# Kernel tuning notes

Hardware: AMD Instinct MI355X
Metric: run time of the kernel (lower is better)

The kernel has to match this reference:

```python
import jax, jax.numpy as jnp
import numpy as np

N = 50000      # nodes
E = 800000     # edges (before self-loops)
V = 50000      # vocab
D = 128        # embed_dim
H = 128        # hidden_dim
G = 64         # graphs in batch


def setup_inputs() -> dict:
    key = jax.random.key(0)
    ks = jax.random.split(key, 14)
    x_lex = jax.random.randint(ks[0], (N,), 0, V)
    edge_index = jax.random.randint(ks[1], (2, E), 0, N)
    batch = jnp.sort(jax.random.randint(ks[2], (N,), 0, G))
    s = 1.0 / np.sqrt(D)
    emb = jax.random.normal(ks[3], (V, D), dtype=jnp.float32) * s
    W1 = jax.random.normal(ks[4], (D, H), dtype=jnp.float32) * s
    att_src1 = jax.random.normal(ks[5], (H,), dtype=jnp.float32) * s
    att_dst1 = jax.random.normal(ks[6], (H,), dtype=jnp.float32) * s
    b1 = jnp.zeros((H,), dtype=jnp.float32)
    W2 = jax.random.normal(ks[7], (H, H), dtype=jnp.float32) * s
    att_src2 = jax.random.normal(ks[8], (H,), dtype=jnp.float32) * s
    att_dst2 = jax.random.normal(ks[9], (H,), dtype=jnp.float32) * s
    b2 = jnp.zeros((H,), dtype=jnp.float32)
    Wc = jax.random.normal(ks[10], (H, 1), dtype=jnp.float32) * s
    bc = jnp.zeros((1,), dtype=jnp.float32)
    return dict(x_lex=x_lex, edge_index=edge_index, batch=batch, emb=emb,
                W1=W1, att_src1=att_src1, att_dst1=att_dst1, b1=b1,
                W2=W2, att_src2=att_src2, att_dst2=att_dst2, b2=b2,
                Wc=Wc, bc=bc)


def _gat_conv(x, src, dst, W, a_src, a_dst, b):
    # PyG GATConv, heads=1, self-loops already appended to src/dst.
    h = x @ W                                   # [N, H]
    e = jax.nn.leaky_relu((h @ a_src)[src] + (h @ a_dst)[dst], 0.2)  # [Etot]
    m = jax.ops.segment_max(e, dst, num_segments=N)
    p = jnp.exp(e - m[dst])
    z = jax.ops.segment_sum(p, dst, num_segments=N)
    alpha = p / z[dst]                          # softmax per destination node
    out = jax.ops.segment_sum(alpha[:, None] * h[src], dst, num_segments=N)
    return out + b


def reference(x_lex, edge_index, batch, emb, W1, att_src1, att_dst1, b1,
              W2, att_src2, att_dst2, b2, Wc, bc):
    loops = jnp.arange(N, dtype=edge_index.dtype)
    src = jnp.concatenate([edge_index[0], loops])   # add self-loops (PyG default)
    dst = jnp.concatenate([edge_index[1], loops])
    x = emb[x_lex]                                  # [N, D]
    h = jax.nn.relu(_gat_conv(x, src, dst, W1, att_src1, att_dst1, b1))
    h = jax.nn.relu(_gat_conv(h, src, dst, W2, att_src2, att_dst2, b2))
    sums = jax.ops.segment_sum(h, batch, num_segments=G)           # [G, H]
    cnt = jax.ops.segment_sum(jnp.ones((N,), h.dtype), batch, num_segments=G)
    h_pool = sums / jnp.maximum(cnt, 1.0)[:, None]
    logits = h_pool @ Wc + bc                                       # [G, 1]
    return (logits, h_pool)
```

## Files before the change

kernel.cpp:

```cpp
#include <hip/hip_runtime.h>
#include <hip/hip_bf16.h>


#define THREADS 256
#define PSLICE 16
#define BUK_S 196
#define SORT_BLOCKS 128

typedef __attribute__((ext_vector_type(8))) short short8v;
typedef __attribute__((ext_vector_type(4))) float f32x4;

static __device__ __forceinline__ unsigned short f2bf(float f) {
    unsigned int u = __float_as_uint(f);
    return (unsigned short)((u + 0x7fffu + ((u >> 16) & 1u)) >> 16);
}
static __device__ __forceinline__ float bf2f(unsigned short b) {
    return __uint_as_float(((unsigned int)b) << 16);
}

__global__ __launch_bounds__(THREADS) void k_prep(const float* __restrict__ W1,
                                                  const float* __restrict__ W2,
                                                  unsigned short* __restrict__ Wh1,
                                                  unsigned short* __restrict__ Wl1,
                                                  unsigned short* __restrict__ Wh2,
                                                  unsigned short* __restrict__ Wl2,
                                                  int* __restrict__ bcount, int nbuk) {
    if (blockIdx.x == 0 && threadIdx.x < nbuk) bcount[threadIdx.x] = 0;
    int t = blockIdx.x * THREADS + threadIdx.x;
    const float* W = W1;
    unsigned short* Wh = Wh1;
    unsigned short* Wl = Wl1;
    if (t >= 128 * 128) {
        t -= 128 * 128;
        W = W2; Wh = Wh2; Wl = Wl2;
    }
    int k = t >> 7, n = t & 127;
    float w = W[t];
    unsigned short h = f2bf(w);
    unsigned short lo = f2bf(w - bf2f(h));
    int c = n >> 4, nl = n & 15, tt = k >> 5, kk = k & 31, g = kk >> 3, j = kk & 7;
    int o = (((c * 4 + tt) * 64) + g * 16 + nl) * 8 + j;
    Wh[o] = h;
    Wl[o] = lo;
}

__global__ __launch_bounds__(THREADS) void k_bukhist(const int* __restrict__ dst,
                                                     int* __restrict__ bcount, int E_, int chunk) {
    __shared__ int hist[THREADS];
    hist[threadIdx.x] = 0;
    __syncthreads();
    int e0 = blockIdx.x * chunk;
    int e1 = min(e0 + chunk, E_);
    for (int e = e0 + threadIdx.x; e < e1; e += THREADS)
        atomicAdd(&hist[dst[e] / BUK_S], 1);
    __syncthreads();
    int c = hist[threadIdx.x];
    if (c) atomicAdd(&bcount[threadIdx.x], c);
}

__global__ __launch_bounds__(THREADS) void k_bukscan(const int* __restrict__ bcount,
                                                     int* __restrict__ sbase,
                                                     int* __restrict__ gcur,
                                                     int* __restrict__ cbase,
                                                     int nbuk, int Nn) {
    __shared__ int s[THREADS];
    int tid = threadIdx.x;
    int v = (tid < nbuk) ? bcount[tid] : 0;
    s[tid] = v;
    __syncthreads();
    for (int off = 1; off < THREADS; off <<= 1) {
        int t = (tid >= off) ? s[tid - off] : 0;
        __syncthreads();
        s[tid] += t;
        __syncthreads();
    }
    int excl1 = s[tid] - v;
    if (tid < nbuk) { sbase[tid] = excl1; gcur[tid] = excl1; }
    int n0 = tid * BUK_S;
    int ns = (tid < nbuk) ? min(BUK_S, Nn - n0) : 0;
    int v2 = v + ns;
    __syncthreads();
    s[tid] = v2;
    __syncthreads();
    for (int off = 1; off < THREADS; off <<= 1) {
        int t = (tid >= off) ? s[tid - off] : 0;
        __syncthreads();
        s[tid] += t;
        __syncthreads();
    }
    if (tid < nbuk) cbase[tid] = s[tid] - v2;
}

__global__ __launch_bounds__(THREADS) void k_bukscatter(const int* __restrict__ src,
                                                        const int* __restrict__ dst,
                                                        int* __restrict__ gcur,
                                                        unsigned int* __restrict__ rec,
                                                        int E_, int chunk) {
    __shared__ int hist[THREADS];
    __shared__ int base[THREADS];
    hist[threadIdx.x] = 0;
    __syncthreads();
    int e0 = blockIdx.x * chunk;
    int e1 = min(e0 + chunk, E_);
    for (int e = e0 + threadIdx.x; e < e1; e += THREADS)
        atomicAdd(&hist[dst[e] / BUK_S], 1);
    __syncthreads();
    int c = hist[threadIdx.x];
    if (c) base[threadIdx.x] = atomicAdd(&gcur[threadIdx.x], c);
    hist[threadIdx.x] = 0;
    __syncthreads();
    for (int e = e0 + threadIdx.x; e < e1; e += THREADS) {
        int d = dst[e];
        int b = d / BUK_S;
        int r = atomicAdd(&hist[b], 1);
        rec[base[b] + r] = (unsigned int)src[e] | ((unsigned int)(d - b * BUK_S) << 17);
    }
}

__global__ __launch_bounds__(THREADS) void k_csr(const unsigned int* __restrict__ rec,
                                                 const int* __restrict__ sbase,
                                                 const int* __restrict__ bcount,
                                                 const int* __restrict__ cbase,
                                                 int* __restrict__ rowptr,
                                                 int* __restrict__ esrc,
                                                 int Nn, int nbuk, int Etot) {
    __shared__ int cnt[THREADS];
    __shared__ int s[THREADS];
    __shared__ int cur[THREADS];
    int b = blockIdx.x;
    int tid = threadIdx.x;
    int n0 = b * BUK_S;
    int ns = min(BUK_S, Nn - n0);
    int cnt_e = bcount[b];
    int rbase = sbase[b];
    int cb = cbase[b];

    cnt[tid] = 0;
    __syncthreads();
    for (int i = tid; i < cnt_e; i += THREADS)
        atomicAdd(&cnt[rec[rbase + i] >> 17], 1);
    __syncthreads();
    int v = (tid < ns) ? cnt[tid] + 1 : 0;
    s[tid] = v;
    __syncthreads();
    for (int off = 1; off < THREADS; off <<= 1) {
        int t = (tid >= off) ? s[tid - off] : 0;
        __syncthreads();
        s[tid] += t;
        __syncthreads();
    }
    int excl = s[tid] - v;
    __syncthreads();
    s[tid] = excl;
    cur[tid] = excl;
    if (tid < ns) rowptr[n0 + tid] = cb + excl;
    if (b == nbuk - 1 && tid == 0) rowptr[Nn] = Etot;
    __syncthreads();
    for (int i = tid; i < cnt_e; i += THREADS) {
        unsigned int r = rec[rbase + i];
        int l = r >> 17;
        int slot = atomicAdd(&cur[l], 1);
        esrc[cb + slot] = (int)(r & 0x1FFFFu);
    }
    __syncthreads();
    if (tid < ns) esrc[cb + s[tid] + cnt[tid]] = n0 + tid;
}

static __device__ __forceinline__ int xsw(int r, int c) {
    return (((r * 16 + (c >> 3)) ^ (r & 7)) << 3) | (c & 7);
}

__global__ __launch_bounds__(THREADS) void k_gemm(const float* __restrict__ X,
                                                  const int* __restrict__ idx,
                                                  const unsigned short* __restrict__ WBh,
                                                  const unsigned short* __restrict__ WBl,
                                                  const float* __restrict__ a_s,
                                                  const float* __restrict__ a_d,
                                                  unsigned short* __restrict__ outb,
                                                  float* __restrict__ as_,
                                                  float* __restrict__ ad_, int Nrows) {
    __shared__ unsigned short xh[64 * 128];

    {
        int r = threadIdx.x >> 2;
        int c0 = (threadIdx.x & 3) * 32;
        int R = blockIdx.x * 64 + r;
        if (R < Nrows) {
            int g = idx ? idx[R] : R;
            const float4* xrow = (const float4*)(X + (size_t)g * 128);
            #pragma unroll
            for (int i = 0; i < 8; ++i) {
                float4 v = xrow[(c0 >> 2) + i];
                ushort4 hh;
                hh.x = f2bf(v.x);
                hh.y = f2bf(v.y);
                hh.z = f2bf(v.z);
                hh.w = f2bf(v.w);
                *(ushort4*)&xh[xsw(r, c0 + i * 4)] = hh;
            }
        } else {
            #pragma unroll
            for (int i = 0; i < 8; ++i)
                *(ushort4*)&xh[xsw(r, c0 + i * 4)] = make_ushort4(0, 0, 0, 0);
        }
    }
    __syncthreads();

    int wid = threadIdx.x >> 6;
    int lane = threadIdx.x & 63;
    int nl = lane & 15;
    int g = lane >> 4;
    int arow = wid * 16 + nl;

    f32x4 acc[8];
    #pragma unroll
    for (int c = 0; c < 8; ++c) acc[c] = (f32x4){0.f, 0.f, 0.f, 0.f};

    #pragma unroll
    for (int t = 0; t < 4; ++t) {
        short8v ah = *(const short8v*)&xh[xsw(arow, t * 32 + g * 8)];
        #pragma unroll
        for (int c = 0; c < 8; ++c) {
            int bo = (((c * 4 + t) * 64) + lane) * 8;
            short8v bh = *(const short8v*)&WBh[bo];
            short8v bl = *(const short8v*)&WBl[bo];
            acc[c] = __builtin_amdgcn_mfma_f32_16x16x32_bf16(ah, bh, acc[c], 0, 0, 0);
            acc[c] = __builtin_amdgcn_mfma_f32_16x16x32_bf16(ah, bl, acc[c], 0, 0, 0);
        }
    }

    float asv[8], adv[8];
    #pragma unroll
    for (int c = 0; c < 8; ++c) {
        asv[c] = a_s[c * 16 + nl];
        adv[c] = a_d[c * 16 + nl];
    }
    int Rb = blockIdx.x * 64 + wid * 16 + g * 4;
    #pragma unroll
    for (int r = 0; r < 4; ++r) {
        int R = Rb + r;
        bool ok = (R < Nrows);
        float ps = 0.f, pd = 0.f;
        #pragma unroll
        for (int c = 0; c < 8; ++c) {
            float v = acc[c][r];
            if (ok) outb[(size_t)R * 128 + c * 16 + nl] = f2bf(v);
            ps = fmaf(v, asv[c], ps);
            pd = fmaf(v, adv[c], pd);
        }
        #pragma unroll
        for (int o = 8; o; o >>= 1) {
            ps += __shfl_xor(ps, o);
            pd += __shfl_xor(pd, o);
        }
        if (ok && nl == 0) {
            as_[R] = ps;
            ad_[R] = pd;
        }
    }
}

__global__ __launch_bounds__(THREADS) void k_agg(const unsigned short* __restrict__ hb,
                                                 const float* __restrict__ as_,
                                                 const float* __restrict__ ad_,
                                                 const int* __restrict__ rowptr,
                                                 const int* __restrict__ esrc,
                                                 const float* __restrict__ bias,
                                                 float* __restrict__ out, int Nn) {
    __shared__ int2 ep[4][64];
    int w = threadIdx.x >> 6;
    int lane = threadIdx.x & 63;
    int half = lane >> 5;
    int j = lane & 31;
    int d = blockIdx.x * 4 + w;
    if (d >= Nn) return;
    int beg = rowptr[d], end = rowptr[d + 1];
    float adv = ad_[d];
    float z = 0.f, a0 = 0.f, a1 = 0.f, a2 = 0.f, a3 = 0.f;
    for (int c0 = beg; c0 < end; c0 += 64) {
        int kk = c0 + lane;
        bool ok = (kk < end);
        int sl = esrc[ok ? kk : beg];
        float pv = 0.f;
        if (ok) {
            float e = as_[sl] + adv;
            e = (e > 0.f) ? e : 0.2f * e;
            pv = __expf(e);
        }
        ep[w][lane] = make_int2(sl, __float_as_int(pv));
        int cn = end - c0;
        if (cn > 64) cn = 64;
        for (int k0 = 0; k0 < cn; k0 += 16) {
            int2 ev[8];
            #pragma unroll
            for (int i = 0; i < 8; ++i)
                ev[i] = ep[w][(k0 + 2 * i + half) & 63];
            uint2 hv[8];
            #pragma unroll
            for (int i = 0; i < 8; ++i)
                hv[i] = *(const uint2*)&hb[((size_t)ev[i].x << 7) + j * 4];
            #pragma unroll
            for (int i = 0; i < 8; ++i) {
                float p = __int_as_float(ev[i].y);
                z += p;
                a0 += p * __uint_as_float(hv[i].x << 16);
                a1 += p * __uint_as_float(hv[i].x & 0xffff0000u);
                a2 += p * __uint_as_float(hv[i].y << 16);
                a3 += p * __uint_as_float(hv[i].y & 0xffff0000u);
            }
        }
    }
    z  += __shfl_xor(z, 32);
    a0 += __shfl_xor(a0, 32);
    a1 += __shfl_xor(a1, 32);
    a2 += __shfl_xor(a2, 32);
    a3 += __shfl_xor(a3, 32);
    if (half == 0) {
        float inv = 1.f / z;
        float4 o;
        o.x = fmaxf(a0 * inv + bias[j * 4 + 0], 0.f);
        o.y = fmaxf(a1 * inv + bias[j * 4 + 1], 0.f);
        o.z = fmaxf(a2 * inv + bias[j * 4 + 2], 0.f);
        o.w = fmaxf(a3 * inv + bias[j * 4 + 3], 0.f);
        *(float4*)&out[(size_t)d * 128 + j * 4] = o;
    }
}

__global__ __launch_bounds__(THREADS) void k_pool_partial(const float* __restrict__ x,
                                                          const int* __restrict__ batch,
                                                          float* __restrict__ part, int Nn) {
    int g = blockIdx.x;
    int s = blockIdx.y;
    int a = 0, b = Nn;
    while (a < b) { int mid = (a + b) >> 1; if (batch[mid] < g) a = mid + 1; else b = mid; }
    int lo = a;
    b = Nn;
    while (a < b) { int mid = (a + b) >> 1; if (batch[mid] < g + 1) a = mid + 1; else b = mid; }
    int hi = a;

    int j = threadIdx.x & 127;
    int half = threadIdx.x >> 7;
    float acc = 0.f;
    for (int n = lo + s * 2 + half; n < hi; n += 2 * PSLICE) acc += x[(size_t)n * 128 + j];
    __shared__ float sred[THREADS];
    sred[threadIdx.x] = acc;
    __syncthreads();
    if (half == 0) part[((size_t)g * PSLICE + s) * 128 + j] = sred[j] + sred[128 + j];
}

__global__ __launch_bounds__(128) void k_pool_final(const float* __restrict__ part,
                                                    const int* __restrict__ batch,
                                                    const float* __restrict__ Wc,
                                                    const float* __restrict__ bc,
                                                    float* __restrict__ out, int Nn, int Gn) {
    int g = blockIdx.x;
    int j = threadIdx.x;
    int a = 0, b = Nn;
    while (a < b) { int mid = (a + b) >> 1; if (batch[mid] < g) a = mid + 1; else b = mid; }
    int lo = a;
    b = Nn;
    while (a < b) { int mid = (a + b) >> 1; if (batch[mid] < g + 1) a = mid + 1; else b = mid; }
    int cnt = a - lo;

    float s = 0.f;
    #pragma unroll
    for (int t = 0; t < PSLICE; ++t) s += part[((size_t)g * PSLICE + t) * 128 + j];
    float mean = s / fmaxf((float)cnt, 1.f);
    out[Gn + (size_t)g * 128 + j] = mean;

    __shared__ float sred[128];
    sred[j] = mean * Wc[j];
    __syncthreads();
    for (int off = 64; off >= 1; off >>= 1) {
        if (j < off) sred[j] += sred[j + off];
        __syncthreads();
    }
    if (j == 0) out[g] = sred[0] + bc[0];
}

static inline size_t align256(size_t x) { return (x + 255) & ~(size_t)255; }

extern "C" void kernel_launch(void* const* d_in, const int* in_sizes, int n_in,
                              void* d_out, int out_size, void* d_ws, size_t ws_size,
                              hipStream_t stream) {
    const int* x_lex = (const int*)d_in[0];
    const int* eidx  = (const int*)d_in[1];
    const int* batch = (const int*)d_in[2];
    const float* emb = (const float*)d_in[3];
    const float* W1  = (const float*)d_in[4];
    const float* a_s1 = (const float*)d_in[5];
    const float* a_d1 = (const float*)d_in[6];
    const float* b1  = (const float*)d_in[7];
    const float* W2  = (const float*)d_in[8];
    const float* a_s2 = (const float*)d_in[9];
    const float* a_d2 = (const float*)d_in[10];
    const float* b2  = (const float*)d_in[11];
    const float* Wc  = (const float*)d_in[12];
    const float* bc  = (const float*)d_in[13];

    const int N = in_sizes[0];
    const int E = in_sizes[1] / 2;
    const int G = out_size / 129;
    const int Etot = E + N;
    const int* esrc_in = eidx;
    const int* edst_in = eidx + E;
    const int NBUK = (N + BUK_S - 1) / BUK_S;

    char* p = (char*)d_ws;
    unsigned short* hb = (unsigned short*)p;  p += align256((size_t)N * 128 * 2);
    float* obuf = (float*)p;            p += align256((size_t)N * 128 * 4);
    float* as_  = (float*)p;            p += align256((size_t)N * 4);
    float* ad_  = (float*)p;            p += align256((size_t)N * 4);
    int* bcount = (int*)p;              p += align256((size_t)NBUK * 4);
    int* sbase  = (int*)p;              p += align256((size_t)NBUK * 4);
    int* gcur   = (int*)p;              p += align256((size_t)NBUK * 4);
    int* cbase  = (int*)p;              p += align256((size_t)NBUK * 4);
    int* rowptr = (int*)p;              p += align256((size_t)(N + 1) * 4);
    unsigned int* rec = (unsigned int*)p; p += align256((size_t)Etot * 4);
    int* esrc   = (int*)p;              p += align256((size_t)Etot * 4);
    float* part = (float*)p;            p += align256((size_t)G * PSLICE * 128 * 4);
    unsigned short* WBh1 = (unsigned short*)p; p += align256((size_t)128 * 128 * 2);
    unsigned short* WBl1 = (unsigned short*)p; p += align256((size_t)128 * 128 * 2);
    unsigned short* WBh2 = (unsigned short*)p; p += align256((size_t)128 * 128 * 2);
    unsigned short* WBl2 = (unsigned short*)p; p += align256((size_t)128 * 128 * 2);

    const int chunk = (E + SORT_BLOCKS - 1) / SORT_BLOCKS;
    const int gemm_grid = (N + 63) / 64;
    const int agg_grid = (N + 3) / 4;

    k_prep<<<128, THREADS, 0, stream>>>(W1, W2, WBh1, WBl1, WBh2, WBl2, bcount, NBUK);

    k_bukhist<<<SORT_BLOCKS, THREADS, 0, stream>>>(edst_in, bcount, E, chunk);
    k_bukscan<<<1, THREADS, 0, stream>>>(bcount, sbase, gcur, cbase, NBUK, N);
    k_bukscatter<<<SORT_BLOCKS, THREADS, 0, stream>>>(esrc_in, edst_in, gcur, rec, E, chunk);
    k_csr<<<NBUK, THREADS, 0, stream>>>(rec, sbase, bcount, cbase, rowptr, esrc, N, NBUK, Etot);

    k_gemm<<<gemm_grid, THREADS, 0, stream>>>(emb, x_lex, WBh1, WBl1, a_s1, a_d1, hb, as_, ad_, N);
    k_agg<<<agg_grid, THREADS, 0, stream>>>(hb, as_, ad_, rowptr, esrc, b1, obuf, N);

    k_gemm<<<gemm_grid, THREADS, 0, stream>>>(obuf, nullptr, WBh2, WBl2, a_s2, a_d2, hb, as_, ad_, N);
    k_agg<<<agg_grid, THREADS, 0, stream>>>(hb, as_, ad_, rowptr, esrc, b2, obuf, N);

    k_pool_partial<<<dim3(G, PSLICE), THREADS, 0, stream>>>(obuf, batch, part, N);
    k_pool_final<<<G, 128, 0, stream>>>(part, batch, Wc, bc, (float*)d_out, N, G);
}
```

Baseline: 175.5 us.

## Fuse bucket histogram into prep, drop scan kernel, widen agg gathers

Each sort block now writes its bucket histogram into a per-block table inside the weight-prep launch. The scatter kernel derives its own deterministic base offsets from that table, and the CSR kernel recomputes the global bucket scan locally, so the separate histogram and scan launches and the global atomics go away. The aggregation kernel switches from 32-lane halves loading 8 bytes each to 16-lane quarters loading 16 bytes per row, which doubles the edges processed per inner step and adds one more shuffle reduction stage. The cost is redundant per-block scan work in the scatter and CSR kernels, plus more accumulator registers in the aggregation kernel.

Measured after the change: 184.4 us. +5.1%, slower.

```diff
diff --git a/kernel.cpp b/kernel.cpp
--- a/kernel.cpp
+++ b/kernel.cpp
@@ -24,9 +24,24 @@
                                                   unsigned short* __restrict__ Wl1,
                                                   unsigned short* __restrict__ Wh2,
                                                   unsigned short* __restrict__ Wl2,
-                                                  int* __restrict__ bcount, int nbuk) {
-    if (blockIdx.x == 0 && threadIdx.x < nbuk) bcount[threadIdx.x] = 0;
-    int t = blockIdx.x * THREADS + threadIdx.x;
+                                                  const int* __restrict__ dst,
+                                                  int* __restrict__ bhist,
+                                                  int E_, int chunk) {
+    int tid = threadIdx.x;
+    if ((int)blockIdx.x >= 128) {
+        int hb = blockIdx.x - 128;
+        __shared__ int hist[THREADS];
+        hist[tid] = 0;
+        __syncthreads();
+        int e0 = hb * chunk;
+        int e1 = min(e0 + chunk, E_);
+        for (int e = e0 + tid; e < e1; e += THREADS)
+            atomicAdd(&hist[dst[e] / BUK_S], 1);
+        __syncthreads();
+        bhist[hb * THREADS + tid] = hist[tid];
+        return;
+    }
+    int t = blockIdx.x * THREADS + tid;
     const float* W = W1;
     unsigned short* Wh = Wh1;
     unsigned short* Wl = Wl1;
@@ -44,29 +59,26 @@
     Wl[o] = lo;
 }
 
-__global__ __launch_bounds__(THREADS) void k_bukhist(const int* __restrict__ dst,
-                                                     int* __restrict__ bcount, int E_, int chunk) {
+__global__ __launch_bounds__(THREADS) void k_bukscatter(const int* __restrict__ src,
+                                                        const int* __restrict__ dst,
+                                                        const int* __restrict__ bhist,
+                                                        int* __restrict__ bcount,
+                                                        unsigned int* __restrict__ rec,
+                                                        int E_, int chunk) {
+    __shared__ int s[THREADS];
+    __shared__ int base[THREADS];
     __shared__ int hist[THREADS];
-    hist[threadIdx.x] = 0;
-    __syncthreads();
-    int e0 = blockIdx.x * chunk;
-    int e1 = min(e0 + chunk, E_);
-    for (int e = e0 + threadIdx.x; e < e1; e += THREADS)
-        atomicAdd(&hist[dst[e] / BUK_S], 1);
-    __syncthreads();
-    int c = hist[threadIdx.x];
-    if (c) atomicAdd(&bcount[threadIdx.x], c);
-}
-
-__global__ __launch_bounds__(THREADS) void k_bukscan(const int* __restrict__ bcount,
-                                                     int* __restrict__ sbase,
-                                                     int* __restrict__ gcur,
-                                                     int* __restrict__ cbase,
-                                                     int nbuk, int Nn) {
-    __shared__ int s[THREADS];
     int tid = threadIdx.x;
-    int v = (tid < nbuk) ? bcount[tid] : 0;
-    s[tid] = v;
+    int b = blockIdx.x;
+    int tot = 0, mypre = 0;
+    #pragma unroll 8
+    for (int bb = 0; bb < SORT_BLOCKS; ++bb) {
+        int v = bhist[bb * THREADS + tid];
+        if (bb < b) mypre += v;
+        tot += v;
+    }
+    if (b == 0) bcount[tid] = tot;
+    s[tid] = tot;
     __syncthreads();
     for (int off = 1; off < THREADS; off <<= 1) {
         int t = (tid >= off) ? s[tid - off] : 0;
@@ -74,74 +86,56 @@
         s[tid] += t;
         __syncthreads();
     }
-    int excl1 = s[tid] - v;
-    if (tid < nbuk) { sbase[tid] = excl1; gcur[tid] = excl1; }
-    int n0 = tid * BUK_S;
-    int ns = (tid < nbuk) ? min(BUK_S, Nn - n0) : 0;
-    int v2 = v + ns;
-    __syncthreads();
-    s[tid] = v2;
-    __syncthreads();
-    for (int off = 1; off < THREADS; off <<= 1) {
-        int t = (tid >= off) ? s[tid - off] : 0;
-        __syncthreads();
-        s[tid] += t;
-        __syncthreads();
-    }
-    if (tid < nbuk) cbase[tid] = s[tid] - v2;
-}
-
-__global__ __launch_bounds__(THREADS) void k_bukscatter(const int* __restrict__ src,
-                                                        const int* __restrict__ dst,
-                                                        int* __restrict__ gcur,
-                                                        unsigned int* __restrict__ rec,
-                                                        int E_, int chunk) {
-    __shared__ int hist[THREADS];
-    __shared__ int base[THREADS];
-    hist[threadIdx.x] = 0;
-    __syncthreads();
-    int e0 = blockIdx.x * chunk;
+    base[tid] = (s[tid] - tot) + mypre;
+    hist[tid] = 0;
+    __syncthreads();
+    int e0 = b * chunk;
     int e1 = min(e0 + chunk, E_);
-    for (int e = e0 + threadIdx.x; e < e1; e += THREADS)
-        atomicAdd(&hist[dst[e] / BUK_S], 1);
-    __syncthreads();
-    int c = hist[threadIdx.x];
-    if (c) base[threadIdx.x] = atomicAdd(&gcur[threadIdx.x], c);
-    hist[threadIdx.x] = 0;
-    __syncthreads();
-    for (int e = e0 + threadIdx.x; e < e1; e += THREADS) {
+    for (int e = e0 + tid; e < e1; e += THREADS) {
         int d = dst[e];
-        int b = d / BUK_S;
-        int r = atomicAdd(&hist[b], 1);
-        rec[base[b] + r] = (unsigned int)src[e] | ((unsigned int)(d - b * BUK_S) << 17);
+        int bk = d / BUK_S;
+        int r = atomicAdd(&hist[bk], 1);
+        rec[base[bk] + r] = (unsigned int)src[e] | ((unsigned int)(d - bk * BUK_S) << 17);
     }
 }
 
 __global__ __launch_bounds__(THREADS) void k_csr(const unsigned int* __restrict__ rec,
-                                                 const int* __restrict__ sbase,
                                                  const int* __restrict__ bcount,
-                                                 const int* __restrict__ cbase,
                                                  int* __restrict__ rowptr,
                                                  int* __restrict__ esrc,
                                                  int Nn, int nbuk, int Etot) {
+    __shared__ int sA[THREADS];
+    __shared__ int lbc[THREADS];
     __shared__ int cnt[THREADS];
     __shared__ int s[THREADS];
     __shared__ int cur[THREADS];
     int b = blockIdx.x;
     int tid = threadIdx.x;
+    int v = (tid < nbuk) ? bcount[tid] : 0;
+    lbc[tid] = v;
+    sA[tid] = v;
+    __syncthreads();
+    for (int off = 1; off < THREADS; off <<= 1) {
+        int t = (tid >= off) ? sA[tid - off] : 0;
+        __syncthreads();
+        sA[tid] += t;
+        __syncthreads();
+    }
+    sA[tid] -= v;
+    __syncthreads();
     int n0 = b * BUK_S;
     int ns = min(BUK_S, Nn - n0);
-    int cnt_e = bcount[b];
-    int rbase = sbase[b];
-    int cb = cbase[b];
+    int cnt_e = lbc[b];
+    int rbase = sA[b];
+    int cb = rbase + b * BUK_S;
 
     cnt[tid] = 0;
     __syncthreads();
     for (int i = tid; i < cnt_e; i += THREADS)
         atomicAdd(&cnt[rec[rbase + i] >> 17], 1);
     __syncthreads();
-    int v = (tid < ns) ? cnt[tid] + 1 : 0;
-    s[tid] = v;
+    int w = (tid < ns) ? cnt[tid] + 1 : 0;
+    s[tid] = w;
     __syncthreads();
     for (int off = 1; off < THREADS; off <<= 1) {
         int t = (tid >= off) ? s[tid - off] : 0;
@@ -149,7 +143,7 @@
         s[tid] += t;
         __syncthreads();
     }
-    int excl = s[tid] - v;
+    int excl = s[tid] - w;
     __syncthreads();
     s[tid] = excl;
     cur[tid] = excl;
@@ -270,13 +264,14 @@
     __shared__ int2 ep[4][64];
     int w = threadIdx.x >> 6;
     int lane = threadIdx.x & 63;
-    int half = lane >> 5;
-    int j = lane & 31;
+    int q = lane >> 4;
+    int j = lane & 15;
     int d = blockIdx.x * 4 + w;
     if (d >= Nn) return;
     int beg = rowptr[d], end = rowptr[d + 1];
     float adv = ad_[d];
-    float z = 0.f, a0 = 0.f, a1 = 0.f, a2 = 0.f, a3 = 0.f;
+    float z = 0.f;
+    float a[8] = {0.f, 0.f, 0.f, 0.f, 0.f, 0.f, 0.f, 0.f};
     for (int c0 = beg; c0 < end; c0 += 64) {
         int kk = c0 + lane;
         bool ok = (kk < end);
@@ -290,39 +285,50 @@
         ep[w][lane] = make_int2(sl, __float_as_int(pv));
         int cn = end - c0;
         if (cn > 64) cn = 64;
-        for (int k0 = 0; k0 < cn; k0 += 16) {
+        for (int k0 = 0; k0 < cn; k0 += 32) {
             int2 ev[8];
             #pragma unroll
             for (int i = 0; i < 8; ++i)
-                ev[i] = ep[w][(k0 + 2 * i + half) & 63];
-            uint2 hv[8];
+                ev[i] = ep[w][(k0 + 4 * i + q) & 63];
+            uint4 hv[8];
             #pragma unroll
             for (int i = 0; i < 8; ++i)
-                hv[i] = *(const uint2*)&hb[((size_t)ev[i].x << 7) + j * 4];
+                hv[i] = *(const uint4*)&hb[((size_t)ev[i].x << 7) + j * 8];
             #pragma unroll
             for (int i = 0; i < 8; ++i) {
                 float p = __int_as_float(ev[i].y);
                 z += p;
-                a0 += p * __uint_as_float(hv[i].x << 16);
-                a1 += p * __uint_as_float(hv[i].x & 0xffff0000u);
-                a2 += p * __uint_as_float(hv[i].y << 16);
-                a3 += p * __uint_as_float(hv[i].y & 0xffff0000u);
+                a[0] += p * __uint_as_float(hv[i].x << 16);
+                a[1] += p * __uint_as_float(hv[i].x & 0xffff0000u);
+                a[2] += p * __uint_as_float(hv[i].y << 16);
+                a[3] += p * __uint_as_float(hv[i].y & 0xffff0000u);
+                a[4] += p * __uint_as_float(hv[i].z << 16);
+                a[5] += p * __uint_as_float(hv[i].z & 0xffff0000u);
+                a[6] += p * __uint_as_float(hv[i].w << 16);
+                a[7] += p * __uint_as_float(hv[i].w & 0xffff0000u);
             }
         }
     }
-    z  += __shfl_xor(z, 32);
-    a0 += __shfl_xor(a0, 32);
-    a1 += __shfl_xor(a1, 32);
-    a2 += __shfl_xor(a2, 32);
-    a3 += __shfl_xor(a3, 32);
-    if (half == 0) {
+    z += __shfl_xor(z, 16);
+    z += __shfl_xor(z, 32);
+    #pragma unroll
+    for (int t = 0; t < 8; ++t) {
+        a[t] += __shfl_xor(a[t], 16);
+        a[t] += __shfl_xor(a[t], 32);
+    }
+    if (q == 0) {
         float inv = 1.f / z;
-        float4 o;
-        o.x = fmaxf(a0 * inv + bias[j * 4 + 0], 0.f);
-        o.y = fmaxf(a1 * inv + bias[j * 4 + 1], 0.f);
-        o.z = fmaxf(a2 * inv + bias[j * 4 + 2], 0.f);
-        o.w = fmaxf(a3 * inv + bias[j * 4 + 3], 0.f);
-        *(float4*)&out[(size_t)d * 128 + j * 4] = o;
+        float4 o1, o2;
+        o1.x = fmaxf(a[0] * inv + bias[j * 8 + 0], 0.f);
+        o1.y = fmaxf(a[1] * inv + bias[j * 8 + 1], 0.f);
+        o1.z = fmaxf(a[2] * inv + bias[j * 8 + 2], 0.f);
+        o1.w = fmaxf(a[3] * inv + bias[j * 8 + 3], 0.f);
+        o2.x = fmaxf(a[4] * inv + bias[j * 8 + 4], 0.f);
+        o2.y = fmaxf(a[5] * inv + bias[j * 8 + 5], 0.f);
+        o2.z = fmaxf(a[6] * inv + bias[j * 8 + 6], 0.f);
+        o2.w = fmaxf(a[7] * inv + bias[j * 8 + 7], 0.f);
+        *(float4*)&out[(size_t)d * 128 + j * 8] = o1;
+        *(float4*)&out[(size_t)d * 128 + j * 8 + 4] = o2;
     }
 }
 
@@ -411,10 +417,8 @@
     float* obuf = (float*)p;            p += align256((size_t)N * 128 * 4);
     float* as_  = (float*)p;            p += align256((size_t)N * 4);
     float* ad_  = (float*)p;            p += align256((size_t)N * 4);
-    int* bcount = (int*)p;              p += align256((size_t)NBUK * 4);
-    int* sbase  = (int*)p;              p += align256((size_t)NBUK * 4);
-    int* gcur   = (int*)p;              p += align256((size_t)NBUK * 4);
-    int* cbase  = (int*)p;              p += align256((size_t)NBUK * 4);
+    int* bhist  = (int*)p;              p += align256((size_t)SORT_BLOCKS * THREADS * 4);
+    int* bcount = (int*)p;              p += align256((size_t)THREADS * 4);
     int* rowptr = (int*)p;              p += align256((size_t)(N + 1) * 4);
     unsigned int* rec = (unsigned int*)p; p += align256((size_t)Etot * 4);
     int* esrc   = (int*)p;              p += align256((size_t)Etot * 4);
@@ -428,12 +432,11 @@
     const int gemm_grid = (N + 63) / 64;
     const int agg_grid = (N + 3) / 4;
 
-    k_prep<<<128, THREADS, 0, stream>>>(W1, W2, WBh1, WBl1, WBh2, WBl2, bcount, NBUK);
-
-    k_bukhist<<<SORT_BLOCKS, THREADS, 0, stream>>>(edst_in, bcount, E, chunk);
-    k_bukscan<<<1, THREADS, 0, stream>>>(bcount, sbase, gcur, cbase, NBUK, N);
-    k_bukscatter<<<SORT_BLOCKS, THREADS, 0, stream>>>(esrc_in, edst_in, gcur, rec, E, chunk);
-    k_csr<<<NBUK, THREADS, 0, stream>>>(rec, sbase, bcount, cbase, rowptr, esrc, N, NBUK, Etot);
+    k_prep<<<128 + SORT_BLOCKS, THREADS, 0, stream>>>(W1, W2, WBh1, WBl1, WBh2, WBl2,
+                                                      edst_in, bhist, E, chunk);
+
+    k_bukscatter<<<SORT_BLOCKS, THREADS, 0, stream>>>(esrc_in, edst_in, bhist, bcount, rec, E, chunk);
+    k_csr<<<NBUK, THREADS, 0, stream>>>(rec, bcount, rowptr, esrc, N, NBUK, Etot);
 
     k_gemm<<<gemm_grid, THREADS, 0, stream>>>(emb, x_lex, WBh1, WBl1, a_s1, a_d1, hb, as_, ad_, N);
     k_agg<<<agg_grid, THREADS, 0, stream>>>(hb, as_, ad_, rowptr, esrc, b1, obuf, N);
```
